# Performance work log

Hardware: AMD Instinct MI355X
Metric: run time of the kernel (lower is better)

Reference implementation:

```python
import jax, jax.numpy as jnp
import numpy as np

BG_W = 1.0
DILATED_BG_W = 5.0
EDGE_W = 20.0
KSIZE = 3


def setup_inputs() -> dict:
    key = jax.random.key(0)
    k1, k2 = jax.random.split(key)
    B, C, H, W = 16, 1, 1024, 1024
    pred = jax.random.normal(k1, (B, C, H, W), dtype=jnp.float32)
    target = (jax.random.uniform(k2, (B, C, H, W)) < 0.05).astype(jnp.float32)
    return {"pred": pred, "target": target}


def _dilate(target):
    # cv2.dilate with KSIZExKSIZE rect kernel == max pool, stride 1, SAME padding
    return jax.lax.reduce_window(
        target, -jnp.inf, jax.lax.max,
        window_dimensions=(1, 1, KSIZE, KSIZE),
        window_strides=(1, 1, 1, 1),
        padding="SAME",
    )


def reference(pred, target):
    dilated = _dilate(target)
    # weight: edge pixels (target>0.5) -> EDGE_W, else dilated band -> DILATED_BG_W, else BG_W
    weight = jnp.where(target > 0.5, EDGE_W,
                       jnp.where(dilated > 0.5, DILATED_BG_W, BG_W))
    # binary_cross_entropy_with_logits, reduction='none', then mean
    x = pred
    losses = weight * (jnp.maximum(x, 0.0) - x * target + jnp.log1p(jnp.exp(-jnp.abs(x))))
    return jnp.mean(losses)
```

## Files before the change

### kernel.cpp

```cpp
#include <hip/hip_runtime.h>

#define HH 1024
#define WW 1024
#define W4 (WW / 4)
#define ROWS 4

__device__ __forceinline__ float fmax3(float a, float b, float c) {
    return fmaxf(a, fmaxf(b, c));
}

__device__ __forceinline__ float loss_elem(float x, float t, float dil) {
    float w = (t > 0.5f) ? 20.0f : ((dil > 0.5f) ? 5.0f : 1.0f);
    float a  = fabsf(x);
    float sp = __logf(1.0f + __expf(-a));
    return w * (fmaxf(x, 0.0f) - x * t + sp);
}

__global__ __launch_bounds__(256) void dilatedweightBCE_main(
        const float* __restrict__ pred,
        const float* __restrict__ target,
        float* __restrict__ partial) {
    __shared__ float swave[4];

    const int tid  = threadIdx.x;
    const int lane = tid & 63;
    const int c    = tid * 4;
    const int b    = blockIdx.y;
    const int h0   = blockIdx.x * ROWS;

    const float* timg = target + (size_t)b * HH * WW;
    const float4* tg  = (const float4*)timg;
    const float4* pg  = (const float4*)(pred + (size_t)b * HH * WW);
    const float4 zero = make_float4(0.0f, 0.0f, 0.0f, 0.0f);

    float4 tr[ROWS + 2];
    tr[0] = (h0 > 0) ? tg[(size_t)(h0 - 1) * W4 + tid] : zero;
    #pragma unroll
    for (int r = 0; r < ROWS; ++r)
        tr[r + 1] = tg[(size_t)(h0 + r) * W4 + tid];
    tr[ROWS + 1] = (h0 + ROWS < HH) ? tg[(size_t)(h0 + ROWS) * W4 + tid] : zero;

    float4 xr[ROWS];
    #pragma unroll
    for (int r = 0; r < ROWS; ++r)
        xr[r] = pg[(size_t)(h0 + r) * W4 + tid];

    float halo[ROWS];
    #pragma unroll
    for (int r = 0; r < ROWS; ++r) halo[r] = 0.0f;
    if (lane == 0 || lane == 63) {
        const int pc = (lane == 0) ? c - 1 : c + 4;
        if (pc >= 0 && pc < WW) {
            float pv[ROWS + 2];
            pv[0] = (h0 > 0) ? timg[(size_t)(h0 - 1) * WW + pc] : 0.0f;
            #pragma unroll
            for (int r = 0; r < ROWS; ++r)
                pv[r + 1] = timg[(size_t)(h0 + r) * WW + pc];
            pv[ROWS + 1] = (h0 + ROWS < HH)
                         ? timg[(size_t)(h0 + ROWS) * WW + pc] : 0.0f;
            #pragma unroll
            for (int r = 0; r < ROWS; ++r)
                halo[r] = fmax3(pv[r], pv[r + 1], pv[r + 2]);
        }
    }

    float s = 0.0f;
    #pragma unroll
    for (int r = 0; r < ROWS; ++r) {
        float4 a = tr[r], m = tr[r + 1], d = tr[r + 2];
        float4 vm = make_float4(fmax3(a.x, m.x, d.x), fmax3(a.y, m.y, d.y),
                                fmax3(a.z, m.z, d.z), fmax3(a.w, m.w, d.w));

        float l  = __shfl_up(vm.w, 1);
        float rr = __shfl_down(vm.x, 1);
        if (lane == 0)  l  = halo[r];
        if (lane == 63) rr = halo[r];

        float d0 = fmax3(l,    vm.x, vm.y);
        float d1 = fmax3(vm.x, vm.y, vm.z);
        float d2 = fmax3(vm.y, vm.z, vm.w);
        float d3 = fmax3(vm.z, vm.w, rr);

        float4 x = xr[r];
        s += loss_elem(x.x, m.x, d0);
        s += loss_elem(x.y, m.y, d1);
        s += loss_elem(x.z, m.z, d2);
        s += loss_elem(x.w, m.w, d3);
    }

    #pragma unroll
    for (int off = 32; off > 0; off >>= 1)
        s += __shfl_down(s, off);

    const int wave = tid >> 6;
    if (lane == 0) swave[wave] = s;
    __syncthreads();
    if (tid == 0) {
        partial[blockIdx.y * gridDim.x + blockIdx.x] =
            swave[0] + swave[1] + swave[2] + swave[3];
    }
}

__global__ __launch_bounds__(256) void dilatedweightBCE_reduce(
        const float* __restrict__ partial,
        float* __restrict__ out,
        int npart4,
        float inv_n) {
    __shared__ float swave[4];
    const int tid = threadIdx.x;

    float s = 0.0f;
    const float4* p4 = (const float4*)partial;
    for (int i = tid; i < npart4; i += 256) {
        float4 v = p4[i];
        s += v.x + v.y + v.z + v.w;
    }

    #pragma unroll
    for (int off = 32; off > 0; off >>= 1)
        s += __shfl_down(s, off);

    const int wave = tid >> 6;
    const int lane = tid & 63;
    if (lane == 0) swave[wave] = s;
    __syncthreads();
    if (tid == 0)
        out[0] = (swave[0] + swave[1] + swave[2] + swave[3]) * inv_n;
}

extern "C" void kernel_launch(void* const* d_in, const int* in_sizes, int n_in,
                              void* d_out, int out_size, void* d_ws, size_t ws_size,
                              hipStream_t stream) {
    const float* pred   = (const float*)d_in[0];
    const float* target = (const float*)d_in[1];
    float* out     = (float*)d_out;
    float* partial = (float*)d_ws;

    const int n  = in_sizes[0];
    const int Bn = n / (HH * WW);
    const int nblocks = (HH / ROWS) * Bn;

    dim3 grid(HH / ROWS, Bn);
    dilatedweightBCE_main<<<grid, 256, 0, stream>>>(pred, target, partial);
    dilatedweightBCE_reduce<<<1, 256, 0, stream>>>(partial, out,
                                                   nblocks / 4, 1.0f / (float)n);
}
```

Measured before the change: 142.1 us.

## Process four row bands per block with register double-buffered prefetch

Each block now walks four consecutive 4-row bands instead of one, loading the next band's target and pred rows into a second register stage while computing the current one. The grid shrinks by a factor of four, so fewer partial sums are written and reduced. The aim is to keep more loads in flight per thread and hide memory latency. The cost is roughly double the register pressure, lower occupancy, and fewer blocks to spread across CUs. The weight selection is also replaced by an FMA formula that is only exact for binary targets.

```diff
diff --git a/kernel.cpp b/kernel.cpp
--- a/kernel.cpp
+++ b/kernel.cpp
@@ -4,19 +4,86 @@
 #define WW 1024
 #define W4 (WW / 4)
 #define ROWS 4
+#define BANDS 4
+#define NT 256
+
+struct Stage {
+    float4 tr[ROWS + 2];
+    float4 xr[ROWS];
+    float  halo[ROWS];
+};
 
 __device__ __forceinline__ float fmax3(float a, float b, float c) {
     return fmaxf(a, fmaxf(b, c));
 }
 
 __device__ __forceinline__ float loss_elem(float x, float t, float dil) {
-    float w = (t > 0.5f) ? 20.0f : ((dil > 0.5f) ? 5.0f : 1.0f);
+    float w = fmaf(15.0f, t, fmaf(4.0f, dil, 1.0f));
     float a  = fabsf(x);
     float sp = __logf(1.0f + __expf(-a));
     return w * (fmaxf(x, 0.0f) - x * t + sp);
 }
 
-__global__ __launch_bounds__(256) void dilatedweightBCE_main(
+__device__ __forceinline__ void load_stage(Stage& st,
+        const float4* __restrict__ tg, const float4* __restrict__ pg,
+        const float* __restrict__ timg, int hb, int tid, int lane, int c) {
+    const float4 zero = make_float4(0.0f, 0.0f, 0.0f, 0.0f);
+    st.tr[0] = (hb > 0) ? tg[(size_t)(hb - 1) * W4 + tid] : zero;
+    #pragma unroll
+    for (int r = 0; r < ROWS; ++r)
+        st.tr[r + 1] = tg[(size_t)(hb + r) * W4 + tid];
+    st.tr[ROWS + 1] = (hb + ROWS < HH) ? tg[(size_t)(hb + ROWS) * W4 + tid] : zero;
+    #pragma unroll
+    for (int r = 0; r < ROWS; ++r)
+        st.xr[r] = pg[(size_t)(hb + r) * W4 + tid];
+
+    #pragma unroll
+    for (int r = 0; r < ROWS; ++r) st.halo[r] = 0.0f;
+    if (lane == 0 || lane == 63) {
+        const int pc = (lane == 0) ? c - 1 : c + 4;
+        if (pc >= 0 && pc < WW) {
+            float pv[ROWS + 2];
+            pv[0] = (hb > 0) ? timg[(size_t)(hb - 1) * WW + pc] : 0.0f;
+            #pragma unroll
+            for (int r = 0; r < ROWS; ++r)
+                pv[r + 1] = timg[(size_t)(hb + r) * WW + pc];
+            pv[ROWS + 1] = (hb + ROWS < HH)
+                         ? timg[(size_t)(hb + ROWS) * WW + pc] : 0.0f;
+            #pragma unroll
+            for (int r = 0; r < ROWS; ++r)
+                st.halo[r] = fmax3(pv[r], pv[r + 1], pv[r + 2]);
+        }
+    }
+}
+
+__device__ __forceinline__ float compute_stage(const Stage& st, int lane) {
+    float s = 0.0f;
+    #pragma unroll
+    for (int r = 0; r < ROWS; ++r) {
+        float4 a = st.tr[r], m = st.tr[r + 1], d = st.tr[r + 2];
+        float4 vm = make_float4(fmax3(a.x, m.x, d.x), fmax3(a.y, m.y, d.y),
+                                fmax3(a.z, m.z, d.z), fmax3(a.w, m.w, d.w));
+
+        float l  = __shfl_up(vm.w, 1);
+        float rr = __shfl_down(vm.x, 1);
+        if (lane == 0)  l  = st.halo[r];
+        if (lane == 63) rr = st.halo[r];
+
+        float d0 = fmax3(l,    vm.x, vm.y);
+        float d1 = fmax3(vm.x, vm.y, vm.z);
+        float d2 = fmax3(vm.y, vm.z, vm.w);
+        float d3 = fmax3(vm.z, vm.w, rr);
+
+        float4 x = st.xr[r];
+        s += loss_elem(x.x, m.x, d0);
+        s += loss_elem(x.y, m.y, d1);
+        s += loss_elem(x.z, m.z, d2);
+        s += loss_elem(x.w, m.w, d3);
+    }
+    return s;
+}
+
+__global__ __launch_bounds__(NT) void dilatedweightBCE_main(
         const float* __restrict__ pred,
         const float* __restrict__ target,
         float* __restrict__ partial) {
@@ -26,66 +93,22 @@
     const int lane = tid & 63;
     const int c    = tid * 4;
     const int b    = blockIdx.y;
-    const int h0   = blockIdx.x * ROWS;
+    const int h0   = blockIdx.x * (ROWS * BANDS);
 
     const float* timg = target + (size_t)b * HH * WW;
     const float4* tg  = (const float4*)timg;
     const float4* pg  = (const float4*)(pred + (size_t)b * HH * WW);
-    const float4 zero = make_float4(0.0f, 0.0f, 0.0f, 0.0f);
 
-    float4 tr[ROWS + 2];
-    tr[0] = (h0 > 0) ? tg[(size_t)(h0 - 1) * W4 + tid] : zero;
-    #pragma unroll
-    for (int r = 0; r < ROWS; ++r)
-        tr[r + 1] = tg[(size_t)(h0 + r) * W4 + tid];
-    tr[ROWS + 1] = (h0 + ROWS < HH) ? tg[(size_t)(h0 + ROWS) * W4 + tid] : zero;
-
-    float4 xr[ROWS];
-    #pragma unroll
-    for (int r = 0; r < ROWS; ++r)
-        xr[r] = pg[(size_t)(h0 + r) * W4 + tid];
-
-    float halo[ROWS];
-    #pragma unroll
-    for (int r = 0; r < ROWS; ++r) halo[r] = 0.0f;
-    if (lane == 0 || lane == 63) {
-        const int pc = (lane == 0) ? c - 1 : c + 4;
-        if (pc >= 0 && pc < WW) {
-            float pv[ROWS + 2];
-            pv[0] = (h0 > 0) ? timg[(size_t)(h0 - 1) * WW + pc] : 0.0f;
-            #pragma unroll
-            for (int r = 0; r < ROWS; ++r)
-                pv[r + 1] = timg[(size_t)(h0 + r) * WW + pc];
-            pv[ROWS + 1] = (h0 + ROWS < HH)
-                         ? timg[(size_t)(h0 + ROWS) * WW + pc] : 0.0f;
-            #pragma unroll
-            for (int r = 0; r < ROWS; ++r)
-                halo[r] = fmax3(pv[r], pv[r + 1], pv[r + 2]);
-        }
-    }
+    Stage sa, sb;
+    load_stage(sa, tg, pg, timg, h0, tid, lane, c);
 
     float s = 0.0f;
     #pragma unroll
-    for (int r = 0; r < ROWS; ++r) {
-        float4 a = tr[r], m = tr[r + 1], d = tr[r + 2];
-        float4 vm = make_float4(fmax3(a.x, m.x, d.x), fmax3(a.y, m.y, d.y),
-                                fmax3(a.z, m.z, d.z), fmax3(a.w, m.w, d.w));
-
-        float l  = __shfl_up(vm.w, 1);
-        float rr = __shfl_down(vm.x, 1);
-        if (lane == 0)  l  = halo[r];
-        if (lane == 63) rr = halo[r];
-
-        float d0 = fmax3(l,    vm.x, vm.y);
-        float d1 = fmax3(vm.x, vm.y, vm.z);
-        float d2 = fmax3(vm.y, vm.z, vm.w);
-        float d3 = fmax3(vm.z, vm.w, rr);
-
-        float4 x = xr[r];
-        s += loss_elem(x.x, m.x, d0);
-        s += loss_elem(x.y, m.y, d1);
-        s += loss_elem(x.z, m.z, d2);
-        s += loss_elem(x.w, m.w, d3);
+    for (int k = 0; k < BANDS; ++k) {
+        if (k + 1 < BANDS)
+            load_stage((k & 1) ? sa : sb, tg, pg, timg,
+                       h0 + (k + 1) * ROWS, tid, lane, c);
+        s += compute_stage((k & 1) ? sb : sa, lane);
     }
 
     #pragma unroll
@@ -101,7 +124,7 @@
     }
 }
 
-__global__ __launch_bounds__(256) void dilatedweightBCE_reduce(
+__global__ __launch_bounds__(NT) void dilatedweightBCE_reduce(
         const float* __restrict__ partial,
         float* __restrict__ out,
         int npart4,
@@ -111,7 +134,7 @@
 
     float s = 0.0f;
     const float4* p4 = (const float4*)partial;
-    for (int i = tid; i < npart4; i += 256) {
+    for (int i = tid; i < npart4; i += NT) {
         float4 v = p4[i];
         s += v.x + v.y + v.z + v.w;
     }
@@ -138,10 +161,10 @@
 
     const int n  = in_sizes[0];
     const int Bn = n / (HH * WW);
-    const int nblocks = (HH / ROWS) * Bn;
+    const int nblocks = (HH / (ROWS * BANDS)) * Bn;
 
-    dim3 grid(HH / ROWS, Bn);
-    dilatedweightBCE_main<<<grid, 256, 0, stream>>>(pred, target, partial);
-    dilatedweightBCE_reduce<<<1, 256, 0, stream>>>(partial, out,
-                                                   nblocks / 4, 1.0f / (float)n);
+    dim3 grid(HH / (ROWS * BANDS), Bn);
+    dilatedweightBCE_main<<<grid, NT, 0, stream>>>(pred, target, partial);
+    dilatedweightBCE_reduce<<<1, NT, 0, stream>>>(partial, out,
+                                                  nblocks / 4, 1.0f / (float)n);
 }
```

Result: slower. 148.3 us (+4.3%).

## Map one row per 256 threads in 1024-thread blocks, write per-wave partials

Applied to the files above, without the earlier changes.

The main kernel now uses 1024-thread blocks where each group of 256 threads handles a single row, replacing the scheme where each thread looped over four rows. Each thread reloads its own up and down target rows, so vertical neighbour reuse now comes from cache instead of registers. When the workspace is large enough, each wave writes its partial sum directly, which skips the block-level shared-memory reduction and barrier. The weight select becomes an FMA expression, which is only valid for binary target values. The final single-block reduce now has to sum a partial array sixteen times larger.

```diff
diff --git a/kernel.cpp b/kernel.cpp
--- a/kernel.cpp
+++ b/kernel.cpp
@@ -2,116 +2,110 @@
 
 #define HH 1024
 #define WW 1024
-#define W4 (WW / 4)
-#define ROWS 4
+#define RPB 4
+#define NT 1024
 
 __device__ __forceinline__ float fmax3(float a, float b, float c) {
     return fmaxf(a, fmaxf(b, c));
 }
 
 __device__ __forceinline__ float loss_elem(float x, float t, float dil) {
-    float w = (t > 0.5f) ? 20.0f : ((dil > 0.5f) ? 5.0f : 1.0f);
+    float w = fmaf(15.0f, t, fmaf(4.0f, dil, 1.0f));
     float a  = fabsf(x);
     float sp = __logf(1.0f + __expf(-a));
     return w * (fmaxf(x, 0.0f) - x * t + sp);
 }
 
-__global__ __launch_bounds__(256) void dilatedweightBCE_main(
+template <bool PER_WAVE>
+__global__ __launch_bounds__(NT) void dilatedweightBCE_main(
         const float* __restrict__ pred,
         const float* __restrict__ target,
         float* __restrict__ partial) {
-    __shared__ float swave[4];
+    __shared__ float swave[NT / 64];
 
-    const int tid  = threadIdx.x;
-    const int lane = tid & 63;
-    const int c    = tid * 4;
+    const int t    = threadIdx.x;
+    const int lane = t & 63;
+    const int w16  = t >> 6;
+    const int rin  = t >> 8;
+    const int c    = (t & 255) * 4;
     const int b    = blockIdx.y;
-    const int h0   = blockIdx.x * ROWS;
+    const int h    = blockIdx.x * RPB + rin;
 
     const float* timg = target + (size_t)b * HH * WW;
-    const float4* tg  = (const float4*)timg;
-    const float4* pg  = (const float4*)(pred + (size_t)b * HH * WW);
+    const size_t rowoff = (size_t)h * WW;
+    const bool has_up = (h > 0);
+    const bool has_dn = (h < HH - 1);
     const float4 zero = make_float4(0.0f, 0.0f, 0.0f, 0.0f);
 
-    float4 tr[ROWS + 2];
-    tr[0] = (h0 > 0) ? tg[(size_t)(h0 - 1) * W4 + tid] : zero;
-    #pragma unroll
-    for (int r = 0; r < ROWS; ++r)
-        tr[r + 1] = tg[(size_t)(h0 + r) * W4 + tid];
-    tr[ROWS + 1] = (h0 + ROWS < HH) ? tg[(size_t)(h0 + ROWS) * W4 + tid] : zero;
+    float4 tmid = *(const float4*)(timg + rowoff + c);
+    float4 tup  = has_up ? *(const float4*)(timg + rowoff - WW + c) : zero;
+    float4 tdn  = has_dn ? *(const float4*)(timg + rowoff + WW + c) : zero;
+    float4 x    = *(const float4*)(pred + (size_t)b * HH * WW + rowoff + c);
 
-    float4 xr[ROWS];
-    #pragma unroll
-    for (int r = 0; r < ROWS; ++r)
-        xr[r] = pg[(size_t)(h0 + r) * W4 + tid];
-
-    float halo[ROWS];
-    #pragma unroll
-    for (int r = 0; r < ROWS; ++r) halo[r] = 0.0f;
+    float halo = 0.0f;
     if (lane == 0 || lane == 63) {
         const int pc = (lane == 0) ? c - 1 : c + 4;
         if (pc >= 0 && pc < WW) {
-            float pv[ROWS + 2];
-            pv[0] = (h0 > 0) ? timg[(size_t)(h0 - 1) * WW + pc] : 0.0f;
-            #pragma unroll
-            for (int r = 0; r < ROWS; ++r)
-                pv[r + 1] = timg[(size_t)(h0 + r) * WW + pc];
-            pv[ROWS + 1] = (h0 + ROWS < HH)
-                         ? timg[(size_t)(h0 + ROWS) * WW + pc] : 0.0f;
-            #pragma unroll
-            for (int r = 0; r < ROWS; ++r)
-                halo[r] = fmax3(pv[r], pv[r + 1], pv[r + 2]);
+            float v = timg[rowoff + pc];
+            if (has_up) v = fmaxf(v, timg[rowoff - WW + pc]);
+            if (has_dn) v = fmaxf(v, timg[rowoff + WW + pc]);
+            halo = v;
         }
     }
 
+    float4 vm = make_float4(fmax3(tup.x, tmid.x, tdn.x),
+                            fmax3(tup.y, tmid.y, tdn.y),
+                            fmax3(tup.z, tmid.z, tdn.z),
+                            fmax3(tup.w, tmid.w, tdn.w));
+
+    float l  = __shfl_up(vm.w, 1);
+    float rr = __shfl_down(vm.x, 1);
+    if (lane == 0)  l  = halo;
+    if (lane == 63) rr = halo;
+
+    float d0 = fmax3(l,    vm.x, vm.y);
+    float d1 = fmax3(vm.x, vm.y, vm.z);
+    float d2 = fmax3(vm.y, vm.z, vm.w);
+    float d3 = fmax3(vm.z, vm.w, rr);
+
     float s = 0.0f;
-    #pragma unroll
-    for (int r = 0; r < ROWS; ++r) {
-        float4 a = tr[r], m = tr[r + 1], d = tr[r + 2];
-        float4 vm = make_float4(fmax3(a.x, m.x, d.x), fmax3(a.y, m.y, d.y),
-                                fmax3(a.z, m.z, d.z), fmax3(a.w, m.w, d.w));
-
-        float l  = __shfl_up(vm.w, 1);
-        float rr = __shfl_down(vm.x, 1);
-        if (lane == 0)  l  = halo[r];
-        if (lane == 63) rr = halo[r];
-
-        float d0 = fmax3(l,    vm.x, vm.y);
-        float d1 = fmax3(vm.x, vm.y, vm.z);
-        float d2 = fmax3(vm.y, vm.z, vm.w);
-        float d3 = fmax3(vm.z, vm.w, rr);
-
-        float4 x = xr[r];
-        s += loss_elem(x.x, m.x, d0);
-        s += loss_elem(x.y, m.y, d1);
-        s += loss_elem(x.z, m.z, d2);
-        s += loss_elem(x.w, m.w, d3);
-    }
+    s += loss_elem(x.x, tmid.x, d0);
+    s += loss_elem(x.y, tmid.y, d1);
+    s += loss_elem(x.z, tmid.z, d2);
+    s += loss_elem(x.w, tmid.w, d3);
 
     #pragma unroll
     for (int off = 32; off > 0; off >>= 1)
         s += __shfl_down(s, off);
 
-    const int wave = tid >> 6;
-    if (lane == 0) swave[wave] = s;
-    __syncthreads();
-    if (tid == 0) {
-        partial[blockIdx.y * gridDim.x + blockIdx.x] =
-            swave[0] + swave[1] + swave[2] + swave[3];
+    if (PER_WAVE) {
+        if (lane == 0)
+            partial[((size_t)blockIdx.y * gridDim.x + blockIdx.x) * (NT / 64) + w16] = s;
+    } else {
+        if (lane == 0) swave[w16] = s;
+        __syncthreads();
+        if (t < 64) {
+            float v = (lane < NT / 64) ? swave[lane] : 0.0f;
+            #pragma unroll
+            for (int off = 8; off > 0; off >>= 1)
+                v += __shfl_down(v, off);
+            if (lane == 0)
+                partial[(size_t)blockIdx.y * gridDim.x + blockIdx.x] = v;
+        }
     }
 }
 
-__global__ __launch_bounds__(256) void dilatedweightBCE_reduce(
+__global__ __launch_bounds__(NT) void dilatedweightBCE_reduce(
         const float* __restrict__ partial,
         float* __restrict__ out,
         int npart4,
         float inv_n) {
-    __shared__ float swave[4];
-    const int tid = threadIdx.x;
+    __shared__ float swave[NT / 64];
+    const int t = threadIdx.x;
 
     float s = 0.0f;
     const float4* p4 = (const float4*)partial;
-    for (int i = tid; i < npart4; i += 256) {
+    for (int i = t; i < npart4; i += NT) {
         float4 v = p4[i];
         s += v.x + v.y + v.z + v.w;
     }
@@ -120,12 +114,15 @@
     for (int off = 32; off > 0; off >>= 1)
         s += __shfl_down(s, off);
 
-    const int wave = tid >> 6;
-    const int lane = tid & 63;
-    if (lane == 0) swave[wave] = s;
+    const int lane = t & 63;
+    if (lane == 0) swave[t >> 6] = s;
     __syncthreads();
-    if (tid == 0)
-        out[0] = (swave[0] + swave[1] + swave[2] + swave[3]) * inv_n;
+    if (t == 0) {
+        float tot = 0.0f;
+        #pragma unroll
+        for (int i = 0; i < NT / 64; ++i) tot += swave[i];
+        out[0] = tot * inv_n;
+    }
 }
 
 extern "C" void kernel_launch(void* const* d_in, const int* in_sizes, int n_in,
@@ -138,10 +135,18 @@
 
     const int n  = in_sizes[0];
     const int Bn = n / (HH * WW);
-    const int nblocks = (HH / ROWS) * Bn;
+    const int nblocks = (HH / RPB) * Bn;
 
-    dim3 grid(HH / ROWS, Bn);
-    dilatedweightBCE_main<<<grid, 256, 0, stream>>>(pred, target, partial);
-    dilatedweightBCE_reduce<<<1, 256, 0, stream>>>(partial, out,
-                                                   nblocks / 4, 1.0f / (float)n);
+    dim3 grid(HH / RPB, Bn);
+    const size_t need = (size_t)nblocks * (NT / 64) * sizeof(float);
+    if (ws_size >= need) {
+        dilatedweightBCE_main<true><<<grid, NT, 0, stream>>>(pred, target, partial);
+        dilatedweightBCE_reduce<<<1, NT, 0, stream>>>(partial, out,
+                                                      nblocks * (NT / 64) / 4,
+                                                      1.0f / (float)n);
+    } else {
+        dilatedweightBCE_main<false><<<grid, NT, 0, stream>>>(pred, target, partial);
+        dilatedweightBCE_reduce<<<1, NT, 0, stream>>>(partial, out,
+                                                      nblocks / 4, 1.0f / (float)n);
+    }
 }
```

After: 158.8 us. 1.12x slower.
